# Performance work log

Hardware: AMD Instinct MI355X
Metric: run time of the kernel (lower is better)

## Reference

```python
import jax, jax.numpy as jnp
import numpy as np
import math

B, S, D, H, R = 4, 2048, 512, 8, 8  # R = k+1 relative slots per direction


def setup_inputs() -> dict:
    key = jax.random.key(0)
    ks = jax.random.split(key, 16)
    dk = D // H
    sc = 1.0 / math.sqrt(D)
    return {
        "query": jax.random.normal(ks[0], (B, S, D), jnp.float32),
        "key": jax.random.normal(ks[1], (B, S, D), jnp.float32),
        "value": jax.random.normal(ks[2], (B, S, D), jnp.float32),
        "start_nodes": jax.random.randint(ks[3], (B, H, R, S), 0, S, jnp.int64 if jax.config.jax_enable_x64 else jnp.int32),
        "end_nodes": jax.random.randint(ks[4], (B, H, R, S), 0, S, jnp.int64 if jax.config.jax_enable_x64 else jnp.int32),
        "rel_q": jax.random.normal(ks[5], (1, H, 2 * R, dk), jnp.float32),
        "rel_k": jax.random.normal(ks[6], (1, H, 2 * R, dk), jnp.float32),
        "rel_v": jax.random.normal(ks[7], (1, H, 2 * R, dk), jnp.float32),
        "Wq": jax.random.normal(ks[8], (D, D), jnp.float32) * sc,
        "bq": jnp.zeros((D,), jnp.float32),
        "Wk": jax.random.normal(ks[9], (D, D), jnp.float32) * sc,
        "bk": jnp.zeros((D,), jnp.float32),
        "Wv": jax.random.normal(ks[10], (D, D), jnp.float32) * sc,
        "bv": jnp.zeros((D,), jnp.float32),
        "Wo": jax.random.normal(ks[11], (D, D), jnp.float32) * sc,
        "bo": jnp.zeros((D,), jnp.float32),
    }


def reference(query, key, value, start_nodes, end_nodes, rel_q, rel_k, rel_v,
              Wq, bq, Wk, bk, Wv, bv, Wo, bo):
    Bs, Ss, Ds = query.shape
    Hs = start_nodes.shape[1]
    dk = Ds // Hs

    def proj(x, W, b):
        return (x @ W.T + b).reshape(Bs, Ss, Hs, dk).transpose(0, 2, 1, 3)  # [B,H,S,dk]

    q = proj(query, Wq, bq)
    k = proj(key, Wk, bk)
    v = proj(value, Wv, bv)

    start_mask = start_nodes == -1
    sn = jnp.where(start_mask, 0, start_nodes)  # -1 padding -> 0 (masked out below)
    qidx = jnp.concatenate([end_nodes, sn], axis=2)  # [B,H,2R,S]
    kidx = jnp.concatenate([sn, end_nodes], axis=2)

    bi = jnp.arange(Bs)[:, None, None, None]
    hi = jnp.arange(Hs)[None, :, None, None]
    q_ctx = q[bi, hi, qidx]  # [B,H,2R,S,dk]
    k_ctx = k[bi, hi, kidx]
    v_ctx = v[bi, hi, kidx]

    # c2c + c2p + p2c, scale_factor = 3 (rel_q and rel_k both provided)
    scores = ((q_ctx * k_ctx).sum(-1)
              + (q_ctx * rel_k[:, :, :, None, :]).sum(-1)
              + (rel_q[:, :, :, None, :] * k_ctx).sum(-1))
    scores = scores / (3.0 * jnp.sqrt(jnp.asarray(dk, scores.dtype)))

    # mask: padded edges masked in both halves; first S flat entries always masked
    mask = jnp.concatenate([start_mask, start_mask], axis=2).reshape(Bs, Hs, -1)
    mask = mask.at[:, :, :Ss].set(True)
    sflat = jnp.exp(jnp.where(mask, -1e9, scores.reshape(Bs, Hs, -1)))  # [B,H,2R*S]

    qf = qidx.reshape(Bs, Hs, -1)
    b2 = jnp.arange(Bs)[:, None, None]
    h2 = jnp.arange(Hs)[None, :, None]
    # scatter-add softmax denominator over destination nodes, then gather back
    denom = jnp.zeros((Bs, Hs, Ss), sflat.dtype).at[b2, h2, qf].add(sflat)
    denom = jnp.where(denom == 0, -1e9, denom)
    probs = (sflat / denom[b2, h2, qf]).reshape(Bs, Hs, -1, Ss, 1)  # [B,H,2R,S,1]

    attn_v = probs * (v_ctx + rel_v[:, :, :, None, :])  # [B,H,2R,S,dk]
    out = jnp.zeros((Bs, Hs, Ss, dk), attn_v.dtype).at[b2, h2, qf].add(
        attn_v.reshape(Bs, Hs, -1, dk))  # scatter-add aggregation over edges

    out = out.transpose(0, 2, 1, 3).reshape(Bs, Ss, Ds)
    return out @ Wo.T + bo
```

## Files before the change

### kernel.cpp

```cpp
#include <hip/hip_runtime.h>
#include <math.h>

#define B_ 4
#define S_ 2048
#define D_ 512
#define H_ 8
#define R_ 8
#define DK_ 64
#define NEDGE (B_*H_*2*R_*S_)
#define EPB   (2*R_*S_)
#define ELLCAP 64

typedef __attribute__((ext_vector_type(8))) short bf16x8;
typedef __attribute__((ext_vector_type(8))) unsigned short ushort8_t;
typedef __attribute__((ext_vector_type(4))) float f32x4;

#define AS1q const __attribute__((address_space(1)))
#define AS3q __attribute__((address_space(3)))

__device__ inline unsigned short f2bf(float f) {
    unsigned u = __builtin_bit_cast(unsigned, f);
    u += 0x7fffu + ((u >> 16) & 1u);
    return (unsigned short)(u >> 16);
}
__device__ inline float bf2f(unsigned short u) {
    return __builtin_bit_cast(float, ((unsigned)u) << 16);
}

__global__ __launch_bounds__(256) void prep(
    const float* __restrict__ query, const float* __restrict__ key,
    const float* __restrict__ value,
    const float* __restrict__ Wq, const float* __restrict__ Wk,
    const float* __restrict__ Wv, const float* __restrict__ Wo,
    const float* __restrict__ rel_q, const float* __restrict__ rel_k,
    const float* __restrict__ rel_v,
    unsigned short* __restrict__ qc, unsigned short* __restrict__ kc,
    unsigned short* __restrict__ vc,
    unsigned short* __restrict__ wqb, unsigned short* __restrict__ wkb,
    unsigned short* __restrict__ wvb, unsigned short* __restrict__ wob,
    unsigned short* __restrict__ rqb, unsigned short* __restrict__ rkb,
    unsigned short* __restrict__ rvb)
{
    int bid = blockIdx.x;
    const float* x;
    unsigned short* y;
    size_t i;
    if (bid < 12288) {
        int z = bid >> 12;
        x = (z == 0) ? query : (z == 1) ? key : value;
        y = (z == 0) ? qc : (z == 1) ? kc : vc;
        i = ((size_t)(bid & 4095) * 256 + threadIdx.x) * 4;
    } else if (bid < 13312) {
        int r = bid - 12288;
        int z = r >> 8;
        x = (z == 0) ? Wq : (z == 1) ? Wk : (z == 2) ? Wv : Wo;
        y = (z == 0) ? wqb : (z == 1) ? wkb : (z == 2) ? wvb : wob;
        i = ((size_t)(r & 255) * 256 + threadIdx.x) * 4;
    } else {
        int r = bid - 13312;
        int z = r >> 3;
        x = (z == 0) ? rel_q : (z == 1) ? rel_k : rel_v;
        y = (z == 0) ? rqb : (z == 1) ? rkb : rvb;
        i = ((size_t)(r & 7) * 256 + threadIdx.x) * 4;
    }
    float4 v = *(const float4*)&x[i];
    *(ushort4*)&y[i] = make_ushort4(f2bf(v.x), f2bf(v.y), f2bf(v.z), f2bf(v.w));
}

template<int TN>
__global__ __launch_bounds__(256) void gemm_bf16(
    const unsigned short* __restrict__ A0, const unsigned short* __restrict__ A1,
    const unsigned short* __restrict__ A2,
    const unsigned short* __restrict__ W0, const unsigned short* __restrict__ W1,
    const unsigned short* __restrict__ W2,
    const float* __restrict__ bi0, const float* __restrict__ bi1, const float* __restrict__ bi2,
    unsigned short* __restrict__ C0, unsigned short* __restrict__ C1,
    unsigned short* __restrict__ C2,
    float* __restrict__ Cf, int a_bhsd)
{
    constexpr int NFR = TN / 32;
    __shared__ unsigned short As[128 * 64];
    __shared__ unsigned short Bs[TN * 64];
    const int z = blockIdx.z;
    const unsigned short* A = (z == 0) ? A0 : (z == 1) ? A1 : A2;
    const unsigned short* W = (z == 0) ? W0 : (z == 1) ? W1 : W2;
    const float* bias        = (z == 0) ? bi0 : (z == 1) ? bi1 : bi2;
    unsigned short* C        = (z == 0) ? C0 : (z == 1) ? C1 : C2;

    const int t    = threadIdx.x;
    const int lane = t & 63;
    const int w    = t >> 6;
    const int wm   = w >> 1, wn = w & 1;
    const int m0   = blockIdx.x * 128;
    const int n0   = blockIdx.y * TN;

    const int lr    = lane >> 3;
    const int cglob = (lane & 7) ^ lr;

    f32x4 acc[4][NFR] = {};

    for (int kk = 0; kk < D_; kk += 64) {
        #pragma unroll
        for (int i = 0; i < 4; ++i) {
            int rowl = w * 32 + i * 8;
            int m = m0 + rowl + lr;
            const unsigned short* ga;
            if (a_bhsd) {
                int b = m >> 11, s = m & (S_ - 1), h = kk >> 6;
                ga = A + ((((size_t)b * H_ + h) * S_ + s) << 6) + cglob * 8;
            } else {
                ga = A + (size_t)m * D_ + kk + cglob * 8;
            }
            __builtin_amdgcn_global_load_lds((AS1q unsigned*)ga,
                (AS3q unsigned*)(As + rowl * 64), 16, 0, 0);
        }
        #pragma unroll
        for (int i = 0; i < TN / 32; ++i) {
            int rowl = w * (TN / 4) + i * 8;
            const unsigned short* gb =
                W + (size_t)(n0 + rowl + lr) * D_ + kk + cglob * 8;
            __builtin_amdgcn_global_load_lds((AS1q unsigned*)gb,
                (AS3q unsigned*)(Bs + rowl * 64), 16, 0, 0);
        }
        __syncthreads();

        #pragma unroll
        for (int ks = 0; ks < 64; ks += 32) {
            const int c0 = ks >> 3;
            bf16x8 af[4], bfr[NFR];
            #pragma unroll
            for (int mi = 0; mi < 4; ++mi) {
                int row = wm * 64 + mi * 16 + (lane & 15);
                int cp  = (c0 + (lane >> 4)) ^ (lane & 7);
                af[mi] = *(const bf16x8*)&As[row * 64 + cp * 8];
            }
            #pragma unroll
            for (int nj = 0; nj < NFR; ++nj) {
                int row = wn * (TN / 2) + nj * 16 + (lane & 15);
                int cp  = (c0 + (lane >> 4)) ^ (lane & 7);
                bfr[nj] = *(const bf16x8*)&Bs[row * 64 + cp * 8];
            }
            #pragma unroll
            for (int mi = 0; mi < 4; ++mi)
                #pragma unroll
                for (int nj = 0; nj < NFR; ++nj)
                    acc[mi][nj] = __builtin_amdgcn_mfma_f32_16x16x32_bf16(af[mi], bfr[nj], acc[mi][nj], 0, 0, 0);
        }
        __syncthreads();
    }

    #pragma unroll
    for (int mi = 0; mi < 4; ++mi) {
        #pragma unroll
        for (int nj = 0; nj < NFR; ++nj) {
            #pragma unroll
            for (int r = 0; r < 4; ++r) {
                int m = m0 + wm * 64 + mi * 16 + (lane >> 4) * 4 + r;
                int n = n0 + wn * (TN / 2) + nj * 16 + (lane & 15);
                float val = acc[mi][nj][r] + bias[n];
                if (Cf) {
                    Cf[(size_t)m * D_ + n] = val;
                } else {
                    int b = m >> 11, s = m & (S_ - 1);
                    int h = n >> 6,  d = n & 63;
                    C[((((size_t)b * H_ + h) * S_ + s) << 6) + d] = f2bf(val);
                }
            }
        }
    }
}

__global__ __launch_bounds__(1024) void attn_fused(
    const unsigned short* __restrict__ q, const unsigned short* __restrict__ k_,
    const unsigned short* __restrict__ v_,
    const unsigned short* __restrict__ rel_q, const unsigned short* __restrict__ rel_k,
    const unsigned short* __restrict__ rel_v,
    const int* __restrict__ start_nodes, const int* __restrict__ end_nodes,
    unsigned short* __restrict__ attn)
{
    __shared__ unsigned short ell[128 * ELLCAP];
    __shared__ int cnt[128];
    const int bi  = blockIdx.x;
    const int xcd = bi & 7;
    const int loc = bi >> 3;
    const int bh  = xcd * 4 + (loc >> 4);
    const int dlo = (loc & 15) << 7;
    const int t   = threadIdx.x;

    if (t < 128) cnt[t] = 0;
    __syncthreads();

    const int base_idx = bh * (R_ * S_);
    for (int f = t; f < EPB; f += 1024) {
        int r2 = f >> 11;
        if (r2 == 0) continue;
        int s = f & (S_ - 1);
        int idx = base_idx + (r2 & 7) * S_ + s;
        int sn = start_nodes[idx];
        if (sn == -1) continue;
        int en = end_nodes[idx];
        int dst = (r2 < R_) ? en : sn;
        unsigned rel = (unsigned)(dst - dlo);
        if (rel < 128u) {
            int ki = (r2 < R_) ? sn : en;
            int pos = atomicAdd(&cnt[rel], 1);
            if (pos < ELLCAP)
                ell[(rel << 6) + pos] = (unsigned short)((r2 << 11) | ki);
        }
    }
    __syncthreads();

    const int w    = t >> 6;
    const int lane = t & 63;
    const int grp  = lane >> 3;
    const int sub  = lane & 7;
    const int h    = bh & 7;
    const size_t node_base = ((size_t)bh << 11);

    for (int dd = 0; dd < 8; ++dd) {
        int dl  = dd * 16 + w;
        int dst = dlo + dl;

        ushort8_t q8 = *(const ushort8_t*)&q[((node_base + dst) << 6) + sub * 8];
        float qv[8];
        #pragma unroll
        for (int i = 0; i < 8; ++i) qv[i] = bf2f(q8[i]);

        int n = cnt[dl];
        if (n > ELLCAP) n = ELLCAP;
        int d_all = (int)ell[(dl << 6) + lane];

        float den = 0.f;
        float o[8] = {};
        #pragma unroll 2
        for (int j = 0; j < n; j += 8) {
            int slot = j + grp;
            int d = __shfl(d_all, slot);
            bool valid = slot < n;
            int ki = d & (S_ - 1);
            int r2 = (d >> 11) & 15;
            ushort8_t k8  = *(const ushort8_t*)&k_  [((node_base + ki) << 6) + sub * 8];
            ushort8_t rk8 = *(const ushort8_t*)&rel_k[(((h << 4) + r2) << 6) + sub * 8];
            ushort8_t rq8 = *(const ushort8_t*)&rel_q[(((h << 4) + r2) << 6) + sub * 8];
            float p = 0.f;
            #pragma unroll
            for (int i = 0; i < 8; ++i)
                p = fmaf(bf2f(k8[i]), qv[i] + bf2f(rq8[i]),
                         fmaf(qv[i], bf2f(rk8[i]), p));
            p += __shfl_xor(p, 1);
            p += __shfl_xor(p, 2);
            p += __shfl_xor(p, 4);
            float sf = valid ? __expf(p * (1.0f / 24.0f)) : 0.f;
            ushort8_t v8  = *(const ushort8_t*)&v_  [((node_base + ki) << 6) + sub * 8];
            ushort8_t rv8 = *(const ushort8_t*)&rel_v[(((h << 4) + r2) << 6) + sub * 8];
            den += sf;
            #pragma unroll
            for (int i = 0; i < 8; ++i)
                o[i] = fmaf(sf, bf2f(v8[i]) + bf2f(rv8[i]), o[i]);
        }
        den += __shfl_xor(den, 8); den += __shfl_xor(den, 16); den += __shfl_xor(den, 32);
        #pragma unroll
        for (int i = 0; i < 8; ++i) {
            o[i] += __shfl_xor(o[i], 8);
            o[i] += __shfl_xor(o[i], 16);
            o[i] += __shfl_xor(o[i], 32);
        }
        if (grp == 0) {
            float inv = (den > 0.f) ? 1.0f / den : 0.f;
            ushort8_t r;
            #pragma unroll
            for (int i = 0; i < 8; ++i) r[i] = f2bf(o[i] * inv);
            *(ushort8_t*)&attn[((node_base + dst) << 6) + sub * 8] = r;
        }
    }
}

extern "C" void kernel_launch(void* const* d_in, const int* in_sizes, int n_in,
                              void* d_out, int out_size, void* d_ws, size_t ws_size,
                              hipStream_t stream) {
    const float* query = (const float*)d_in[0];
    const float* key   = (const float*)d_in[1];
    const float* value = (const float*)d_in[2];
    const int* start_nodes = (const int*)d_in[3];
    const int* end_nodes   = (const int*)d_in[4];
    const float* rel_q = (const float*)d_in[5];
    const float* rel_k = (const float*)d_in[6];
    const float* rel_v = (const float*)d_in[7];
    const float* Wq = (const float*)d_in[8];
    const float* bq = (const float*)d_in[9];
    const float* Wk = (const float*)d_in[10];
    const float* bk = (const float*)d_in[11];
    const float* Wv = (const float*)d_in[12];
    const float* bv = (const float*)d_in[13];
    const float* Wo = (const float*)d_in[14];
    const float* bo = (const float*)d_in[15];
    float* out = (float*)d_out;

    const size_t NQ = (size_t)B_ * H_ * S_ * DK_;
    const size_t NW = (size_t)D_ * D_;
    const size_t NR = (size_t)H_ * 2 * R_ * DK_;
    unsigned short* p = (unsigned short*)d_ws;
    unsigned short* qc = p;            p += NQ;
    unsigned short* kc = p;            p += NQ;
    unsigned short* vc = p;            p += NQ;
    unsigned short* q  = p;            p += NQ;
    unsigned short* k  = p;            p += NQ;
    unsigned short* v  = p;            p += NQ;
    unsigned short* attn = p;          p += NQ;
    unsigned short* wqb = p;           p += NW;
    unsigned short* wkb = p;           p += NW;
    unsigned short* wvb = p;           p += NW;
    unsigned short* wob = p;           p += NW;
    unsigned short* rqb = p;           p += NR;
    unsigned short* rkb = p;           p += NR;
    unsigned short* rvb = p;           p += NR;

    prep<<<13336, 256, 0, stream>>>(query, key, value, Wq, Wk, Wv, Wo,
                                    rel_q, rel_k, rel_v,
                                    qc, kc, vc, wqb, wkb, wvb, wob,
                                    rqb, rkb, rvb);

    dim3 ggrid(B_ * S_ / 128, D_ / 128, 3);
    gemm_bf16<128><<<ggrid, 256, 0, stream>>>(qc, kc, vc, wqb, wkb, wvb, bq, bk, bv,
                                              q, k, v, nullptr, 0);

    attn_fused<<<512, 1024, 0, stream>>>(q, k, v, rqb, rkb, rvb,
                                         start_nodes, end_nodes, attn);

    dim3 ogrid(B_ * S_ / 128, D_ / 64, 1);
    gemm_bf16<64><<<ogrid, 256, 0, stream>>>(attn, attn, attn, wob, wob, wob, bo, bo, bo,
                                             nullptr, nullptr, nullptr, out, 1);
}
```

Measured before the change: 218.8 us.

## Fuse activation bf16 conversion into QKV GEMM and keep projections in fp32

Removes the separate pass that converted query/key/value to bf16 and instead converts fp32 activations to bf16 inside the QKV GEMM's global-to-LDS load. The Q/K/V projections are now stored as fp32 and rel_q/k/v are read directly as fp32 in the attention kernel. GEMM blocks are remapped so consecutive rows land on the same XCD. This saves a full read and write of the inputs, but the attention kernel's gathers now read twice as many bytes per edge, and the GEMM A-load goes through registers instead of direct-to-LDS loads.

Measured after the change: 237.0 us. +8.3%, slower.

```diff
diff --git a/kernel.cpp b/kernel.cpp
--- a/kernel.cpp
+++ b/kernel.cpp
@@ -7,7 +7,6 @@
 #define H_ 8
 #define R_ 8
 #define DK_ 64
-#define NEDGE (B_*H_*2*R_*S_)
 #define EPB   (2*R_*S_)
 #define ELLCAP 64
 
@@ -23,100 +22,65 @@
     u += 0x7fffu + ((u >> 16) & 1u);
     return (unsigned short)(u >> 16);
 }
-__device__ inline float bf2f(unsigned short u) {
-    return __builtin_bit_cast(float, ((unsigned)u) << 16);
-}
-
-__global__ __launch_bounds__(256) void prep(
-    const float* __restrict__ query, const float* __restrict__ key,
-    const float* __restrict__ value,
+
+__global__ __launch_bounds__(256) void prep_w(
     const float* __restrict__ Wq, const float* __restrict__ Wk,
     const float* __restrict__ Wv, const float* __restrict__ Wo,
-    const float* __restrict__ rel_q, const float* __restrict__ rel_k,
-    const float* __restrict__ rel_v,
-    unsigned short* __restrict__ qc, unsigned short* __restrict__ kc,
-    unsigned short* __restrict__ vc,
     unsigned short* __restrict__ wqb, unsigned short* __restrict__ wkb,
-    unsigned short* __restrict__ wvb, unsigned short* __restrict__ wob,
-    unsigned short* __restrict__ rqb, unsigned short* __restrict__ rkb,
-    unsigned short* __restrict__ rvb)
+    unsigned short* __restrict__ wvb, unsigned short* __restrict__ wob)
 {
     int bid = blockIdx.x;
-    const float* x;
-    unsigned short* y;
-    size_t i;
-    if (bid < 12288) {
-        int z = bid >> 12;
-        x = (z == 0) ? query : (z == 1) ? key : value;
-        y = (z == 0) ? qc : (z == 1) ? kc : vc;
-        i = ((size_t)(bid & 4095) * 256 + threadIdx.x) * 4;
-    } else if (bid < 13312) {
-        int r = bid - 12288;
-        int z = r >> 8;
-        x = (z == 0) ? Wq : (z == 1) ? Wk : (z == 2) ? Wv : Wo;
-        y = (z == 0) ? wqb : (z == 1) ? wkb : (z == 2) ? wvb : wob;
-        i = ((size_t)(r & 255) * 256 + threadIdx.x) * 4;
-    } else {
-        int r = bid - 13312;
-        int z = r >> 3;
-        x = (z == 0) ? rel_q : (z == 1) ? rel_k : rel_v;
-        y = (z == 0) ? rqb : (z == 1) ? rkb : rvb;
-        i = ((size_t)(r & 7) * 256 + threadIdx.x) * 4;
-    }
+    int z = bid >> 8;
+    const float* x = (z == 0) ? Wq : (z == 1) ? Wk : (z == 2) ? Wv : Wo;
+    unsigned short* y = (z == 0) ? wqb : (z == 1) ? wkb : (z == 2) ? wvb : wob;
+    size_t i = ((size_t)(bid & 255) * 256 + threadIdx.x) * 4;
     float4 v = *(const float4*)&x[i];
     *(ushort4*)&y[i] = make_ushort4(f2bf(v.x), f2bf(v.y), f2bf(v.z), f2bf(v.w));
 }
 
-template<int TN>
-__global__ __launch_bounds__(256) void gemm_bf16(
-    const unsigned short* __restrict__ A0, const unsigned short* __restrict__ A1,
-    const unsigned short* __restrict__ A2,
+__global__ __launch_bounds__(256) void gemm_qkv(
+    const float* __restrict__ A0, const float* __restrict__ A1,
+    const float* __restrict__ A2,
     const unsigned short* __restrict__ W0, const unsigned short* __restrict__ W1,
     const unsigned short* __restrict__ W2,
     const float* __restrict__ bi0, const float* __restrict__ bi1, const float* __restrict__ bi2,
-    unsigned short* __restrict__ C0, unsigned short* __restrict__ C1,
-    unsigned short* __restrict__ C2,
-    float* __restrict__ Cf, int a_bhsd)
+    float* __restrict__ C0, float* __restrict__ C1, float* __restrict__ C2)
 {
-    constexpr int NFR = TN / 32;
     __shared__ unsigned short As[128 * 64];
-    __shared__ unsigned short Bs[TN * 64];
-    const int z = blockIdx.z;
-    const unsigned short* A = (z == 0) ? A0 : (z == 1) ? A1 : A2;
+    __shared__ unsigned short Bs[128 * 64];
+    const int bi  = blockIdx.x;
+    const int xcd = bi & 7;
+    const int r   = bi >> 3;
+    const int z   = r >> 5;
+    const int rr  = r & 31;
+    const int m0  = (xcd * 8 + (rr >> 2)) * 128;
+    const int n0  = (rr & 3) * 128;
+
+    const float* A          = (z == 0) ? A0 : (z == 1) ? A1 : A2;
     const unsigned short* W = (z == 0) ? W0 : (z == 1) ? W1 : W2;
-    const float* bias        = (z == 0) ? bi0 : (z == 1) ? bi1 : bi2;
-    unsigned short* C        = (z == 0) ? C0 : (z == 1) ? C1 : C2;
+    const float* bias       = (z == 0) ? bi0 : (z == 1) ? bi1 : bi2;
+    float* C                = (z == 0) ? C0 : (z == 1) ? C1 : C2;
 
     const int t    = threadIdx.x;
     const int lane = t & 63;
     const int w    = t >> 6;
     const int wm   = w >> 1, wn = w & 1;
-    const int m0   = blockIdx.x * 128;
-    const int n0   = blockIdx.y * TN;
-
     const int lr    = lane >> 3;
     const int cglob = (lane & 7) ^ lr;
 
-    f32x4 acc[4][NFR] = {};
+    f32x4 acc[4][4] = {};
 
     for (int kk = 0; kk < D_; kk += 64) {
         #pragma unroll
         for (int i = 0; i < 4; ++i) {
             int rowl = w * 32 + i * 8;
-            int m = m0 + rowl + lr;
-            const unsigned short* ga;
-            if (a_bhsd) {
-                int b = m >> 11, s = m & (S_ - 1), h = kk >> 6;
-                ga = A + ((((size_t)b * H_ + h) * S_ + s) << 6) + cglob * 8;
-            } else {
-                ga = A + (size_t)m * D_ + kk + cglob * 8;
-            }
-            __builtin_amdgcn_global_load_lds((AS1q unsigned*)ga,
-                (AS3q unsigned*)(As + rowl * 64), 16, 0, 0);
-        }
-        #pragma unroll
-        for (int i = 0; i < TN / 32; ++i) {
-            int rowl = w * (TN / 4) + i * 8;
+            const float* ga = A + (size_t)(m0 + rowl + lr) * D_ + kk + cglob * 8;
+            float4 a0 = *(const float4*)ga;
+            float4 a1 = *(const float4*)(ga + 4);
+            ushort8_t c;
+            c[0] = f2bf(a0.x); c[1] = f2bf(a0.y); c[2] = f2bf(a0.z); c[3] = f2bf(a0.w);
+            c[4] = f2bf(a1.x); c[5] = f2bf(a1.y); c[6] = f2bf(a1.z); c[7] = f2bf(a1.w);
+            *(ushort8_t*)&As[(rowl + lr) * 64 + (lane & 7) * 8] = c;
             const unsigned short* gb =
                 W + (size_t)(n0 + rowl + lr) * D_ + kk + cglob * 8;
             __builtin_amdgcn_global_load_lds((AS1q unsigned*)gb,
@@ -127,7 +91,7 @@
         #pragma unroll
         for (int ks = 0; ks < 64; ks += 32) {
             const int c0 = ks >> 3;
-            bf16x8 af[4], bfr[NFR];
+            bf16x8 af[4], bfr[4];
             #pragma unroll
             for (int mi = 0; mi < 4; ++mi) {
                 int row = wm * 64 + mi * 16 + (lane & 15);
@@ -135,15 +99,15 @@
                 af[mi] = *(const bf16x8*)&As[row * 64 + cp * 8];
             }
             #pragma unroll
-            for (int nj = 0; nj < NFR; ++nj) {
-                int row = wn * (TN / 2) + nj * 16 + (lane & 15);
+            for (int nj = 0; nj < 4; ++nj) {
+                int row = wn * 64 + nj * 16 + (lane & 15);
                 int cp  = (c0 + (lane >> 4)) ^ (lane & 7);
                 bfr[nj] = *(const bf16x8*)&Bs[row * 64 + cp * 8];
             }
             #pragma unroll
             for (int mi = 0; mi < 4; ++mi)
                 #pragma unroll
-                for (int nj = 0; nj < NFR; ++nj)
+                for (int nj = 0; nj < 4; ++nj)
                     acc[mi][nj] = __builtin_amdgcn_mfma_f32_16x16x32_bf16(af[mi], bfr[nj], acc[mi][nj], 0, 0, 0);
         }
         __syncthreads();
@@ -152,29 +116,106 @@
     #pragma unroll
     for (int mi = 0; mi < 4; ++mi) {
         #pragma unroll
-        for (int nj = 0; nj < NFR; ++nj) {
-            #pragma unroll
-            for (int r = 0; r < 4; ++r) {
-                int m = m0 + wm * 64 + mi * 16 + (lane >> 4) * 4 + r;
-                int n = n0 + wn * (TN / 2) + nj * 16 + (lane & 15);
-                float val = acc[mi][nj][r] + bias[n];
-                if (Cf) {
-                    Cf[(size_t)m * D_ + n] = val;
-                } else {
-                    int b = m >> 11, s = m & (S_ - 1);
-                    int h = n >> 6,  d = n & 63;
-                    C[((((size_t)b * H_ + h) * S_ + s) << 6) + d] = f2bf(val);
-                }
+        for (int nj = 0; nj < 4; ++nj) {
+            #pragma unroll
+            for (int rg = 0; rg < 4; ++rg) {
+                int m = m0 + wm * 64 + mi * 16 + (lane >> 4) * 4 + rg;
+                int n = n0 + wn * 64 + nj * 16 + (lane & 15);
+                float val = acc[mi][nj][rg] + bias[n];
+                int b = m >> 11, s = m & (S_ - 1);
+                int h = n >> 6,  d = n & 63;
+                C[((((size_t)b * H_ + h) * S_ + s) << 6) + d] = val;
+            }
+        }
+    }
+}
+
+__global__ __launch_bounds__(256) void gemm_out(
+    const unsigned short* __restrict__ A, const unsigned short* __restrict__ W,
+    const float* __restrict__ bias, float* __restrict__ Cf)
+{
+    __shared__ unsigned short As[128 * 64];
+    __shared__ unsigned short Bs[64 * 64];
+    const int bi  = blockIdx.x;
+    const int xcd = bi & 7;
+    const int r   = bi >> 3;
+    const int m0  = (xcd * 8 + (r >> 3)) * 128;
+    const int n0  = (r & 7) * 64;
+
+    const int t    = threadIdx.x;
+    const int lane = t & 63;
+    const int w    = t >> 6;
+    const int wm   = w >> 1, wn = w & 1;
+    const int lr    = lane >> 3;
+    const int cglob = (lane & 7) ^ lr;
+
+    f32x4 acc[4][2] = {};
+
+    for (int kk = 0; kk < D_; kk += 64) {
+        #pragma unroll
+        for (int i = 0; i < 4; ++i) {
+            int rowl = w * 32 + i * 8;
+            int m = m0 + rowl + lr;
+            int b = m >> 11, s = m & (S_ - 1), h = kk >> 6;
+            const unsigned short* ga =
+                A + ((((size_t)b * H_ + h) * S_ + s) << 6) + cglob * 8;
+            __builtin_amdgcn_global_load_lds((AS1q unsigned*)ga,
+                (AS3q unsigned*)(As + rowl * 64), 16, 0, 0);
+        }
+        #pragma unroll
+        for (int i = 0; i < 2; ++i) {
+            int rowl = w * 16 + i * 8;
+            const unsigned short* gb =
+                W + (size_t)(n0 + rowl + lr) * D_ + kk + cglob * 8;
+            __builtin_amdgcn_global_load_lds((AS1q unsigned*)gb,
+                (AS3q unsigned*)(Bs + rowl * 64), 16, 0, 0);
+        }
+        __syncthreads();
+
+        #pragma unroll
+        for (int ks = 0; ks < 64; ks += 32) {
+            const int c0 = ks >> 3;
+            bf16x8 af[4], bfr[2];
+            #pragma unroll
+            for (int mi = 0; mi < 4; ++mi) {
+                int row = wm * 64 + mi * 16 + (lane & 15);
+                int cp  = (c0 + (lane >> 4)) ^ (lane & 7);
+                af[mi] = *(const bf16x8*)&As[row * 64 + cp * 8];
+            }
+            #pragma unroll
+            for (int nj = 0; nj < 2; ++nj) {
+                int row = wn * 32 + nj * 16 + (lane & 15);
+                int cp  = (c0 + (lane >> 4)) ^ (lane & 7);
+                bfr[nj] = *(const bf16x8*)&Bs[row * 64 + cp * 8];
+            }
+            #pragma unroll
+            for (int mi = 0; mi < 4; ++mi)
+                #pragma unroll
+                for (int nj = 0; nj < 2; ++nj)
+                    acc[mi][nj] = __builtin_amdgcn_mfma_f32_16x16x32_bf16(af[mi], bfr[nj], acc[mi][nj], 0, 0, 0);
+        }
+        __syncthreads();
+    }
+
+    #pragma unroll
+    for (int mi = 0; mi < 4; ++mi) {
+        #pragma unroll
+        for (int nj = 0; nj < 2; ++nj) {
+            #pragma unroll
+            for (int rg = 0; rg < 4; ++rg) {
+                int m = m0 + wm * 64 + mi * 16 + (lane >> 4) * 4 + rg;
+                int n = n0 + wn * 32 + nj * 16 + (lane & 15);
+                Cf[(size_t)m * D_ + n] = acc[mi][nj][rg] + bias[n];
             }
         }
     }
 }
 
 __global__ __launch_bounds__(1024) void attn_fused(
-    const unsigned short* __restrict__ q, const unsigned short* __restrict__ k_,
-    const unsigned short* __restrict__ v_,
-    const unsigned short* __restrict__ rel_q, const unsigned short* __restrict__ rel_k,
-    const unsigned short* __restrict__ rel_v,
+    const float* __restrict__ q, const float* __restrict__ k_,
+    const float* __restrict__ v_,
+    const float* __restrict__ rel_q, const float* __restrict__ rel_k,
+    const float* __restrict__ rel_v,
     const int* __restrict__ start_nodes, const int* __restrict__ end_nodes,
     unsigned short* __restrict__ attn)
 {
@@ -221,10 +262,9 @@
         int dl  = dd * 16 + w;
         int dst = dlo + dl;
 
-        ushort8_t q8 = *(const ushort8_t*)&q[((node_base + dst) << 6) + sub * 8];
         float qv[8];
-        #pragma unroll
-        for (int i = 0; i < 8; ++i) qv[i] = bf2f(q8[i]);
+        *(float4*)&qv[0] = *(const float4*)&q[((node_base + dst) << 6) + sub * 8];
+        *(float4*)&qv[4] = *(const float4*)&q[((node_base + dst) << 6) + sub * 8 + 4];
 
         int n = cnt[dl];
         if (n > ELLCAP) n = ELLCAP;
@@ -239,24 +279,31 @@
             bool valid = slot < n;
             int ki = d & (S_ - 1);
             int r2 = (d >> 11) & 15;
-            ushort8_t k8  = *(const ushort8_t*)&k_  [((node_base + ki) << 6) + sub * 8];
-            ushort8_t rk8 = *(const ushort8_t*)&rel_k[(((h << 4) + r2) << 6) + sub * 8];
-            ushort8_t rq8 = *(const ushort8_t*)&rel_q[(((h << 4) + r2) << 6) + sub * 8];
+            size_t koff = ((node_base + ki) << 6) + sub * 8;
+            int roff = (((h << 4) + r2) << 6) + sub * 8;
+            float kv[8], rqv[8], rkv[8], vv[8], rvv[8];
+            *(float4*)&kv[0]  = *(const float4*)&k_[koff];
+            *(float4*)&kv[4]  = *(const float4*)&k_[koff + 4];
+            *(float4*)&rqv[0] = *(const float4*)&rel_q[roff];
+            *(float4*)&rqv[4] = *(const float4*)&rel_q[roff + 4];
+            *(float4*)&rkv[0] = *(const float4*)&rel_k[roff];
+            *(float4*)&rkv[4] = *(const float4*)&rel_k[roff + 4];
             float p = 0.f;
             #pragma unroll
             for (int i = 0; i < 8; ++i)
-                p = fmaf(bf2f(k8[i]), qv[i] + bf2f(rq8[i]),
-                         fmaf(qv[i], bf2f(rk8[i]), p));
+                p = fmaf(kv[i], qv[i] + rqv[i], fmaf(qv[i], rkv[i], p));
             p += __shfl_xor(p, 1);
             p += __shfl_xor(p, 2);
             p += __shfl_xor(p, 4);
             float sf = valid ? __expf(p * (1.0f / 24.0f)) : 0.f;
-            ushort8_t v8  = *(const ushort8_t*)&v_  [((node_base + ki) << 6) + sub * 8];
-            ushort8_t rv8 = *(const ushort8_t*)&rel_v[(((h << 4) + r2) << 6) + sub * 8];
+            *(float4*)&vv[0]  = *(const float4*)&v_[koff];
+            *(float4*)&vv[4]  = *(const float4*)&v_[koff + 4];
+            *(float4*)&rvv[0] = *(const float4*)&rel_v[roff];
+            *(float4*)&rvv[4] = *(const float4*)&rel_v[roff + 4];
             den += sf;
             #pragma unroll
             for (int i = 0; i < 8; ++i)
-                o[i] = fmaf(sf, bf2f(v8[i]) + bf2f(rv8[i]), o[i]);
+                o[i] = fmaf(sf, vv[i] + rvv[i], o[i]);
         }
         den += __shfl_xor(den, 8); den += __shfl_xor(den, 16); den += __shfl_xor(den, 32);
         #pragma unroll
@@ -267,10 +314,10 @@
         }
         if (grp == 0) {
             float inv = (den > 0.f) ? 1.0f / den : 0.f;
-            ushort8_t r;
-            #pragma unroll
-            for (int i = 0; i < 8; ++i) r[i] = f2bf(o[i] * inv);
-            *(ushort8_t*)&attn[((node_base + dst) << 6) + sub * 8] = r;
+            ushort8_t rs;
+            #pragma unroll
+            for (int i = 0; i < 8; ++i) rs[i] = f2bf(o[i] * inv);
+            *(ushort8_t*)&attn[((node_base + dst) << 6) + sub * 8] = rs;
         }
     }
 }
@@ -298,36 +345,22 @@
 
     const size_t NQ = (size_t)B_ * H_ * S_ * DK_;
     const size_t NW = (size_t)D_ * D_;
-    const size_t NR = (size_t)H_ * 2 * R_ * DK_;
-    unsigned short* p = (unsigned short*)d_ws;
-    unsigned short* qc = p;            p += NQ;
-    unsigned short* kc = p;            p += NQ;
-    unsigned short* vc = p;            p += NQ;
-    unsigned short* q  = p;            p += NQ;
-    unsigned short* k  = p;            p += NQ;
-    unsigned short* v  = p;            p += NQ;
-    unsigned short* attn = p;          p += NQ;
-    unsigned short* wqb = p;           p += NW;
-    unsigned short* wkb = p;           p += NW;
-    unsigned short* wvb = p;           p += NW;
-    unsigned short* wob = p;           p += NW;
-    unsigned short* rqb = p;           p += NR;
-    unsigned short* rkb = p;           p += NR;
-    unsigned short* rvb = p;           p += NR;
-
-    prep<<<13336, 256, 0, stream>>>(query, key, value, Wq, Wk, Wv, Wo,
-                                    rel_q, rel_k, rel_v,
-                                    qc, kc, vc, wqb, wkb, wvb, wob,
-                                    rqb, rkb, rvb);
-
-    dim3 ggrid(B_ * S_ / 128, D_ / 128, 3);
-    gemm_bf16<128><<<ggrid, 256, 0, stream>>>(qc, kc, vc, wqb, wkb, wvb, bq, bk, bv,
-                                              q, k, v, nullptr, 0);
-
-    attn_fused<<<512, 1024, 0, stream>>>(q, k, v, rqb, rkb, rvb,
+    float* qf = (float*)d_ws;
+    float* kf = qf + NQ;
+    float* vf = kf + NQ;
+    unsigned short* attn = (unsigned short*)(vf + NQ);
+    unsigned short* wqb  = attn + NQ;
+    unsigned short* wkb  = wqb + NW;
+    unsigned short* wvb  = wkb + NW;
+    unsigned short* wob  = wvb + NW;
+
+    prep_w<<<1024, 256, 0, stream>>>(Wq, Wk, Wv, Wo, wqb, wkb, wvb, wob);
+
+    gemm_qkv<<<768, 256, 0, stream>>>(query, key, value, wqb, wkb, wvb,
+                                      bq, bk, bv, qf, kf, vf);
+
+    attn_fused<<<512, 1024, 0, stream>>>(qf, kf, vf, rel_q, rel_k, rel_v,
                                          start_nodes, end_nodes, attn);
 
-    dim3 ogrid(B_ * S_ / 128, D_ / 64, 1);
-    gemm_bf16<64><<<ogrid, 256, 0, stream>>>(attn, attn, attn, wob, wob, wob, bo, bo, bo,
-                                             nullptr, nullptr, nullptr, out, 1);
-}
+    gemm_out<<<512, 256, 0, stream>>>(attn, wob, bo, out);
+}
```
